# Kernel tuning notes

Hardware: AMD Instinct MI355X
Metric: run time of the kernel (lower is better)

Reference implementation:

```python
import jax, jax.numpy as jnp
import numpy as np
import math

E = 1024   # embedding_size
H = 16     # layer_size (num heads)
DK = 64    # key_size
DH = 64    # head_size
HID = 4096 # hidden_size
B = 2
S = 2048   # context_size
EPS = 1e-5


def layer_norm(x, w, b):
    mu = jnp.mean(x, axis=-1, keepdims=True)
    var = jnp.mean(jnp.square(x - mu), axis=-1, keepdims=True)
    return (x - mu) * jax.lax.rsqrt(var + EPS) * w + b


def setup_inputs() -> dict:
    key = jax.random.key(0)
    ks = jax.random.split(key, 16)
    sE = 1.0 / math.sqrt(E)
    sH = 1.0 / math.sqrt(HID)
    return {
        "embeddings": jax.random.normal(ks[0], (B, S, E), dtype=jnp.float32),
        "Wq": jax.random.uniform(ks[1], (H, E, DK), minval=-sE, maxval=sE, dtype=jnp.float32),
        "bq": jnp.zeros((H, DK), dtype=jnp.float32),
        "Wk": jax.random.uniform(ks[2], (H, E, DK), minval=-sE, maxval=sE, dtype=jnp.float32),
        "bk": jnp.zeros((H, DK), dtype=jnp.float32),
        "Wv": jax.random.uniform(ks[3], (H, E, DH), minval=-sE, maxval=sE, dtype=jnp.float32),
        "bv": jnp.zeros((H, DH), dtype=jnp.float32),
        "ln1_w": jnp.ones((E,), dtype=jnp.float32),
        "ln1_b": jnp.zeros((E,), dtype=jnp.float32),
        "ln2_w": jnp.ones((E,), dtype=jnp.float32),
        "ln2_b": jnp.zeros((E,), dtype=jnp.float32),
        "W1": jax.random.uniform(ks[4], (E, HID), minval=-sE, maxval=sE, dtype=jnp.float32),
        "b1": jnp.zeros((HID,), dtype=jnp.float32),
        "W2": jax.random.uniform(ks[5], (HID, E), minval=-sH, maxval=sH, dtype=jnp.float32),
        "b2": jnp.zeros((E,), dtype=jnp.float32),
    }


def reference(embeddings, Wq, bq, Wk, bk, Wv, bv, ln1_w, ln1_b, ln2_w, ln2_b, W1, b1, W2, b2):
    # NOTE: faithful to source: residual uses the POST-norm activations
    # (embeddings is reassigned to the LayerNorm output before the residual add).
    x = layer_norm(embeddings, ln1_w, ln1_b)            # [B,S,E]
    q = jnp.einsum('bse,hed->bhsd', x, Wq) + bq[:, None, :]
    k = jnp.einsum('bse,hed->bhsd', x, Wk) + bk[:, None, :]
    v = jnp.einsum('bse,hed->bhsd', x, Wv) + bv[:, None, :]
    scores = jnp.einsum('bhsd,bhtd->bhst', q, k) / math.sqrt(DK)  # [B,H,S,S]
    causal = jnp.tril(jnp.ones((S, S), dtype=bool))
    scores = jnp.where(causal, scores, -jnp.inf)
    w = jax.nn.softmax(scores, axis=-1)
    o = jnp.einsum('bhst,bhtd->bhsd', w, v)             # [B,H,S,DH]
    o = jnp.transpose(o, (0, 2, 1, 3)).reshape(B, S, H * DH)  # concat heads
    x = x + o
    y = layer_norm(x, ln2_w, ln2_b)
    h = jax.nn.relu(jnp.einsum('bse,eh->bsh', y, W1) + b1)
    out = y + jnp.einsum('bsh,he->bse', h, W2) + b2
    return out
```

## Files before the change

kernel.cpp:

```cpp
#include <hip/hip_runtime.h>


typedef unsigned short u16;
typedef unsigned int   u32;
typedef __bf16 bf16x8 __attribute__((ext_vector_type(8)));
typedef float  f32x4  __attribute__((ext_vector_type(4)));

#define NEG_INF (-__builtin_inff())

__device__ __forceinline__ u16 f2b(float f) {
  u32 u = __float_as_uint(f);
  u = (u + 0x7fffu + ((u >> 16) & 1u)) >> 16;
  return (u16)u;
}

__device__ __forceinline__ void gload16(const void* g, void* l) {
  __builtin_amdgcn_global_load_lds(
      (const __attribute__((address_space(1))) u32*)g,
      (__attribute__((address_space(3))) u32*)l, 16, 0, 0);
}

__global__ __launch_bounds__(256)
void transpose_bf16_k(const float* __restrict__ in, u16* __restrict__ out,
                      int R, int C) {
  __shared__ float tile[64][65];
  int r0 = blockIdx.x * 64, c0 = blockIdx.y * 64;
  const float* ip = in + (size_t)blockIdx.z * R * C;
  u16* op = out + (size_t)blockIdx.z * C * R;
  int tr = threadIdx.x >> 6, tc = threadIdx.x & 63;
#pragma unroll
  for (int i = 0; i < 16; i++) {
    int r = i * 4 + tr;
    tile[r][tc] = ip[(size_t)(r0 + r) * C + c0 + tc];
  }
  __syncthreads();
#pragma unroll
  for (int i = 0; i < 16; i++) {
    int c = i * 4 + tr;
    op[(size_t)(c0 + c) * R + r0 + tc] = f2b(tile[tc][c]);
  }
}

__global__ __launch_bounds__(256)
void vtrans_k(const u16* __restrict__ vin, u16* __restrict__ vt) {
  __shared__ __align__(16) u16 tile[64][72];
  int s0 = blockIdx.x * 64, bh = blockIdx.y;
  const u16* ip = vin + (size_t)bh * 2048 * 64;
  u16* op = vt + (size_t)bh * 64 * 2048;
  int t = threadIdx.x;
#pragma unroll
  for (int i = 0; i < 2; i++) {
    int idx = i * 256 + t, r = idx >> 3, c = idx & 7;
    *(uint4*)&tile[r][c * 8] = *(const uint4*)(ip + (size_t)(s0 + r) * 64 + c * 8);
  }
  __syncthreads();
#pragma unroll
  for (int i = 0; i < 16; i++) {
    int d = i * 4 + (t >> 6), s = t & 63;
    op[(size_t)d * 2048 + s0 + s] = tile[s][d];
  }
}

__global__ __launch_bounds__(256)
void ln_k(const float* __restrict__ in, const float* __restrict__ in2,
          const float* __restrict__ w, const float* __restrict__ b,
          float* __restrict__ outf, u16* __restrict__ outb) {
  int row = blockIdx.x, t = threadIdx.x;
  const float4* ip = (const float4*)(in + (size_t)row * 1024);
  float4 x = ip[t];
  if (in2) {
    const float4* ip2 = (const float4*)(in2 + (size_t)row * 1024);
    float4 o = ip2[t];
    x.x += o.x; x.y += o.y; x.z += o.z; x.w += o.w;
  }
  float s = x.x + x.y + x.z + x.w;
  float q = x.x * x.x + x.y * x.y + x.z * x.z + x.w * x.w;
#pragma unroll
  for (int m = 32; m; m >>= 1) { s += __shfl_xor(s, m); q += __shfl_xor(q, m); }
  __shared__ float rs[4], rq[4];
  if ((t & 63) == 0) { rs[t >> 6] = s; rq[t >> 6] = q; }
  __syncthreads();
  s = rs[0] + rs[1] + rs[2] + rs[3];
  q = rq[0] + rq[1] + rq[2] + rq[3];
  float mean = s * (1.f / 1024.f);
  float var  = q * (1.f / 1024.f) - mean * mean;
  float rstd = rsqrtf(var + 1e-5f);
  float4 wv = ((const float4*)w)[t];
  float4 bv = ((const float4*)b)[t];
  float4 y;
  y.x = (x.x - mean) * rstd * wv.x + bv.x;
  y.y = (x.y - mean) * rstd * wv.y + bv.y;
  y.z = (x.z - mean) * rstd * wv.z + bv.z;
  y.w = (x.w - mean) * rstd * wv.w + bv.w;
  if (outf) ((float4*)(outf + (size_t)row * 1024))[t] = y;
  ushort4 ub;
  ub.x = f2b(y.x); ub.y = f2b(y.y); ub.z = f2b(y.z); ub.w = f2b(y.w);
  ((ushort4*)(outb + (size_t)row * 1024))[t] = ub;
}

#define EPI_QKV  0
#define EPI_RELU 1
#define EPI_RES  2

template <int EPI>
__global__ __launch_bounds__(256)
void gemm_k(const u16* __restrict__ A, const u16* __restrict__ Bt,
            int K, int lda, int ldbt,
            const float* __restrict__ bias0, const float* __restrict__ bias1,
            const float* __restrict__ bias2, const float* __restrict__ res,
            int ldout, u16* __restrict__ outb, float* __restrict__ outf,
            float* __restrict__ outp) {
  __shared__ __align__(16) u16 As[128 * 64];
  __shared__ __align__(16) u16 Bs[128 * 64];
  int t = threadIdx.x;
  int wave = t >> 6, lane = t & 63, quad = lane >> 4, l16 = lane & 15;
  int x7 = l16 & 7;
  int wm = (wave >> 1) * 64, wn = (wave & 1) * 64;
  int bm = blockIdx.x * 128, bn = blockIdx.y * 128;
  int zoff = blockIdx.z * K;

  const u16* Agl[4];
  const u16* Bgl[4];
#pragma unroll
  for (int i = 0; i < 4; i++) {
    int idx = i * 256 + t, r = idx >> 3, c = (idx & 7) ^ (r & 7);
    Agl[i] = A + (size_t)(bm + r) * lda + zoff + c * 8;
    Bgl[i] = Bt + (size_t)(bn + r) * ldbt + zoff + c * 8;
  }
  u16* Asl = As + t * 8;
  u16* Bsl = Bs + t * 8;

  f32x4 acc[4][4] = {};

  for (int k0 = 0; k0 < K; k0 += 64) {
#pragma unroll
    for (int i = 0; i < 4; i++) {
      gload16(Agl[i] + k0, Asl + i * 2048);
      gload16(Bgl[i] + k0, Bsl + i * 2048);
    }
    __syncthreads();
#pragma unroll
    for (int kc = 0; kc < 2; kc++) {
      bf16x8 af[4], bfr[4];
#pragma unroll
      for (int i = 0; i < 4; i++) {
        int r = wm + i * 16 + l16;
        af[i] = *(const bf16x8*)(As + r * 64 + (((kc * 4 + quad) ^ x7) * 8));
      }
#pragma unroll
      for (int j = 0; j < 4; j++) {
        int r = wn + j * 16 + l16;
        bfr[j] = *(const bf16x8*)(Bs + r * 64 + (((kc * 4 + quad) ^ x7) * 8));
      }
#pragma unroll
      for (int i = 0; i < 4; i++)
#pragma unroll
        for (int j = 0; j < 4; j++)
          acc[i][j] = __builtin_amdgcn_mfma_f32_16x16x32_bf16(af[i], bfr[j],
                                                              acc[i][j], 0, 0, 0);
    }
    __syncthreads();
  }

#pragma unroll
  for (int i = 0; i < 4; i++) {
#pragma unroll
    for (int j = 0; j < 4; j++) {
      int c = bn + wn + j * 16 + l16;
#pragma unroll
      for (int rr = 0; rr < 4; rr++) {
        int r = bm + wm + i * 16 + quad * 4 + rr;
        float v = acc[i][j][rr];
        if (EPI == EPI_QKV) {
          int which = c >> 10, h = (c >> 6) & 15, d = c & 63;
          const float* bp = which == 0 ? bias0 : (which == 1 ? bias1 : bias2);
          v += bp[h * 64 + d];
          int bb = r >> 11, ss = r & 2047;
          outb[((size_t)(which * 32 + bb * 16 + h) * 2048 + ss) * 64 + d] = f2b(v);
        } else if (EPI == EPI_RELU) {
          v += bias0[c];
          v = v > 0.f ? v : 0.f;
          outb[(size_t)r * ldout + c] = f2b(v);
        } else {
          if (blockIdx.z == 0) {
            v += bias0[c] + res[(size_t)r * ldout + c];
            outf[(size_t)r * ldout + c] = v;
          } else {
            outp[(size_t)r * ldout + c] = v;
          }
        }
      }
    }
  }
}

__global__ __launch_bounds__(256)
void reduce_k(float* __restrict__ out, const float* __restrict__ part) {
  int i = blockIdx.x * 256 + threadIdx.x;
  float4 a = ((const float4*)part)[i];
  float4 b = ((float4*)out)[i];
  b.x += a.x; b.y += a.y; b.z += a.z; b.w += a.w;
  ((float4*)out)[i] = b;
}

__global__ __launch_bounds__(512, 4)
void attn_k(const u16* __restrict__ qkv, const u16* __restrict__ vt,
            float* __restrict__ o) {
  int bh = blockIdx.y;
  int Qt = (bh >> 4) ? (15 - (int)blockIdx.x) : (int)blockIdx.x;
  int b = bh >> 4, h = bh & 15;
  const u16* qg = qkv + (size_t)bh * (2048 * 64) + (size_t)Qt * 128 * 64;
  const u16* kg = qkv + (size_t)(32 + bh) * (2048 * 64);
  const u16* vg = vt + (size_t)bh * (64 * 2048);

  __shared__ __align__(16) u16 Qs[128 * 64];
  __shared__ __align__(16) u16 Ks[2][64 * 64];
  __shared__ __align__(16) u16 Vs[2][64 * 64];
  __shared__ __align__(16) u16 Ps[8][16 * 64];

  int t = threadIdx.x;
  int wave = t >> 6, lane = t & 63, quad = lane >> 4, l16 = lane & 15;

  {
#pragma unroll
    for (int i = 0; i < 2; i++) {
      int idx = i * 512 + t, r = idx >> 3, c = (idx & 7) ^ (r & 7);
      gload16(qg + r * 64 + c * 8, Qs + idx * 8);
    }
    int r = t >> 3, c = (t & 7) ^ (r & 7);
    gload16(kg + (size_t)r * 64 + c * 8, Ks[0] + t * 8);
    gload16(vg + (size_t)r * 2048 + c * 8, Vs[0] + t * 8);
  }
  __syncthreads();

  int x7 = l16 & 7;
  bf16x8 qf[2];
  {
    const u16* qr = Qs + (wave * 16 + l16) * 64;
    qf[0] = *(const bf16x8*)(qr + ((quad ^ x7) * 8));
    qf[1] = *(const bf16x8*)(qr + (((4 + quad) ^ x7) * 8));
  }

  f32x4 oacc[4] = {};
  float mo[4] = {NEG_INF, NEG_INF, NEG_INF, NEG_INF};
  float ll[4] = {};
  u16* Pw = Ps[wave];
  int rmin = Qt * 128 + wave * 16;
  int kmax_w = (rmin + 15) >> 6;
  int klast = 2 * Qt + 1;

  for (int kt = 0; kt <= klast; kt++) {
    const u16* ks = Ks[kt & 1];
    const u16* vs = Vs[kt & 1];
    if (kt < klast) {
      int r = t >> 3, c = (t & 7) ^ (r & 7);
      gload16(kg + (size_t)((kt + 1) * 64 + r) * 64 + c * 8, Ks[(kt + 1) & 1] + t * 8);
      gload16(vg + (size_t)r * 2048 + (kt + 1) * 64 + c * 8, Vs[(kt + 1) & 1] + t * 8);
    }
    if (kt <= kmax_w) {
      f32x4 sc[4];
#pragma unroll
      for (int g = 0; g < 4; g++) {
        const u16* kr = ks + (g * 16 + l16) * 64;
        bf16x8 kf0 = *(const bf16x8*)(kr + ((quad ^ x7) * 8));
        bf16x8 kf1 = *(const bf16x8*)(kr + (((4 + quad) ^ x7) * 8));
        f32x4 s = {};
        s = __builtin_amdgcn_mfma_f32_16x16x32_bf16(qf[0], kf0, s, 0, 0, 0);
        s = __builtin_amdgcn_mfma_f32_16x16x32_bf16(qf[1], kf1, s, 0, 0, 0);
        sc[g] = s;
      }
      if (kt * 64 + 63 > rmin) {
#pragma unroll
        for (int g = 0; g < 4; g++) {
          int col = kt * 64 + g * 16 + l16;
#pragma unroll
          for (int rr = 0; rr < 4; rr++) {
            int row = rmin + quad * 4 + rr;
            sc[g][rr] = (col <= row) ? sc[g][rr] * 0.125f : NEG_INF;
          }
        }
      } else {
#pragma unroll
        for (int g = 0; g < 4; g++)
#pragma unroll
          for (int rr = 0; rr < 4; rr++) sc[g][rr] *= 0.125f;
      }
      float al[4], rsum[4];
#pragma unroll
      for (int rr = 0; rr < 4; rr++) {
        float mx = fmaxf(fmaxf(sc[0][rr], sc[1][rr]), fmaxf(sc[2][rr], sc[3][rr]));
        mx = fmaxf(mx, __shfl_xor(mx, 1));
        mx = fmaxf(mx, __shfl_xor(mx, 2));
        mx = fmaxf(mx, __shfl_xor(mx, 4));
        mx = fmaxf(mx, __shfl_xor(mx, 8));
        float mnew = fmaxf(mo[rr], mx);
        al[rr] = __expf(mo[rr] - mnew);
        mo[rr] = mnew;
        rsum[rr] = 0.f;
      }
#pragma unroll
      for (int g = 0; g < 4; g++) {
        int cbase = (g * 16 + l16 + quad * 16) & 63;
#pragma unroll
        for (int rr = 0; rr < 4; rr++) {
          float p = __expf(sc[g][rr] - mo[rr]);
          rsum[rr] += p;
          Pw[(quad * 4 + rr) * 64 + cbase] = f2b(p);
        }
      }
#pragma unroll
      for (int rr = 0; rr < 4; rr++) {
        rsum[rr] += __shfl_xor(rsum[rr], 1);
        rsum[rr] += __shfl_xor(rsum[rr], 2);
        rsum[rr] += __shfl_xor(rsum[rr], 4);
        rsum[rr] += __shfl_xor(rsum[rr], 8);
        ll[rr] = ll[rr] * al[rr] + rsum[rr];
      }
#pragma unroll
      for (int g = 0; g < 4; g++)
#pragma unroll
        for (int rr = 0; rr < 4; rr++) oacc[g][rr] *= al[rr];
      bf16x8 pf0, pf1;
      {
        const u16* pr = Pw + l16 * 64;
        int sh = (l16 & 12) * 4;
        pf0 = *(const bf16x8*)(pr + ((quad * 8 + sh) & 63));
        pf1 = *(const bf16x8*)(pr + ((32 + quad * 8 + sh) & 63));
      }
#pragma unroll
      for (int g = 0; g < 4; g++) {
        const u16* vr = vs + (g * 16 + l16) * 64;
        bf16x8 vf0 = *(const bf16x8*)(vr + ((quad ^ x7) * 8));
        bf16x8 vf1 = *(const bf16x8*)(vr + (((4 + quad) ^ x7) * 8));
        oacc[g] = __builtin_amdgcn_mfma_f32_16x16x32_bf16(pf0, vf0, oacc[g], 0, 0, 0);
        oacc[g] = __builtin_amdgcn_mfma_f32_16x16x32_bf16(pf1, vf1, oacc[g], 0, 0, 0);
      }
    }
    __syncthreads();
  }

#pragma unroll
  for (int g = 0; g < 4; g++)
#pragma unroll
    for (int rr = 0; rr < 4; rr++) {
      int srow = rmin + quad * 4 + rr;
      o[((size_t)b * 2048 + srow) * 1024 + h * 64 + g * 16 + l16] =
          oacc[g][rr] / ll[rr];
    }
}

extern "C" void kernel_launch(void* const* d_in, const int* in_sizes, int n_in,
                              void* d_out, int out_size, void* d_ws, size_t ws_size,
                              hipStream_t stream) {
  const float* emb  = (const float*)d_in[0];
  const float* Wq   = (const float*)d_in[1];
  const float* bq   = (const float*)d_in[2];
  const float* Wk   = (const float*)d_in[3];
  const float* bk   = (const float*)d_in[4];
  const float* Wv   = (const float*)d_in[5];
  const float* bv   = (const float*)d_in[6];
  const float* ln1w = (const float*)d_in[7];
  const float* ln1b = (const float*)d_in[8];
  const float* ln2w = (const float*)d_in[9];
  const float* ln2b = (const float*)d_in[10];
  const float* W1   = (const float*)d_in[11];
  const float* b1   = (const float*)d_in[12];
  const float* W2   = (const float*)d_in[13];
  const float* b2   = (const float*)d_in[14];
  float* out = (float*)d_out;

  char* p = (char*)d_ws;
  u16*   Wqkv_t = (u16*)p;   p += (size_t)3072 * 1024 * 2;
  u16*   W1t    = (u16*)p;   p += (size_t)4096 * 1024 * 2;
  u16*   W2t    = (u16*)p;   p += (size_t)1024 * 4096 * 2;
  float* x      = (float*)p; p += (size_t)4096 * 1024 * 4;
  u16*   xb     = (u16*)p;   p += (size_t)4096 * 1024 * 2;
  u16*   qkvb   = (u16*)p;   p += (size_t)3 * 32 * 2048 * 64 * 2;
  float* ob     = (float*)p; p += (size_t)4096 * 1024 * 4;
  float* y      = (float*)p; p += (size_t)4096 * 1024 * 4;
  u16*   yb     = (u16*)p;   p += (size_t)4096 * 1024 * 2;
  u16*   hb     = (u16*)qkvb;
  u16*   vT     = (u16*)y;
  float* part   = x;
  if (ws_size < (size_t)(p - (char*)d_ws)) return;

  transpose_bf16_k<<<dim3(16, 1, 16), 256, 0, stream>>>(Wq, Wqkv_t,                   1024, 64);
  transpose_bf16_k<<<dim3(16, 1, 16), 256, 0, stream>>>(Wk, Wqkv_t + 1024 * 1024,     1024, 64);
  transpose_bf16_k<<<dim3(16, 1, 16), 256, 0, stream>>>(Wv, Wqkv_t + 2 * 1024 * 1024, 1024, 64);
  transpose_bf16_k<<<dim3(16, 64, 1), 256, 0, stream>>>(W1, W1t, 1024, 4096);
  transpose_bf16_k<<<dim3(64, 16, 1), 256, 0, stream>>>(W2, W2t, 4096, 1024);

  ln_k<<<dim3(4096), 256, 0, stream>>>(emb, nullptr, ln1w, ln1b, x, xb);

  gemm_k<EPI_QKV><<<dim3(32, 24, 1), 256, 0, stream>>>(
      xb, Wqkv_t, 1024, 1024, 1024, bq, bk, bv, nullptr, 0, qkvb, nullptr, nullptr);

  vtrans_k<<<dim3(32, 32), 256, 0, stream>>>(qkvb + (size_t)64 * 2048 * 64, vT);

  attn_k<<<dim3(16, 32), 512, 0, stream>>>(qkvb, vT, ob);

  ln_k<<<dim3(4096), 256, 0, stream>>>(x, ob, ln2w, ln2b, y, yb);

  gemm_k<EPI_RELU><<<dim3(32, 32, 1), 256, 0, stream>>>(
      yb, W1t, 1024, 1024, 1024, b1, nullptr, nullptr, nullptr, 4096, hb, nullptr, nullptr);

  gemm_k<EPI_RES><<<dim3(32, 8, 2), 256, 0, stream>>>(
      hb, W2t, 2048, 4096, 4096, b2, nullptr, nullptr, y, 1024, nullptr, out, part);

  reduce_k<<<dim3(4096), 256, 0, stream>>>(out, part);
}
```

Baseline: 359.4 us.

## Restructure attention to read K/V directly from global with transposed score tiles

The attention kernel drops the shared-memory double-buffered K/V staging and block-wide barriers. Each 16-row wave now loads Q, K and V fragments straight from global memory, relying on cache reuse. Scores are computed transposed (K as the A operand), so row max and sum need only two cross-lane shuffles, and exp2 is used with the softmax scale times log2(e) folded into the Q projection epilogue. Blocks shrink to 64 query rows and 256 threads over a larger grid, which adds redundant global/L2 traffic for K/V in exchange for no LDS staging or synchronisation.

```diff
diff --git a/kernel.cpp b/kernel.cpp
--- a/kernel.cpp
+++ b/kernel.cpp
@@ -8,6 +8,12 @@
 
 #define NEG_INF (-__builtin_inff())
 
+#if __has_builtin(__builtin_amdgcn_exp2f)
+#define EXP2F(x) __builtin_amdgcn_exp2f(x)
+#else
+#define EXP2F(x) exp2f(x)
+#endif
+
 __device__ __forceinline__ u16 f2b(float f) {
   u32 u = __float_as_uint(f);
   u = (u + 0x7fffu + ((u >> 16) & 1u)) >> 16;
@@ -19,6 +25,8 @@
       (const __attribute__((address_space(1))) u32*)g,
       (__attribute__((address_space(3))) u32*)l, 16, 0, 0);
 }
+
+__device__ __forceinline__ bf16x8 ld16(const u16* p) { return *(const bf16x8*)p; }
 
 __global__ __launch_bounds__(256)
 void transpose_bf16_k(const float* __restrict__ in, u16* __restrict__ out,
@@ -102,6 +110,8 @@
 #define EPI_RELU 1
 #define EPI_RES  2
 
+#define QSCALE 0.18033688011112042f
+
 template <int EPI>
 __global__ __launch_bounds__(256)
 void gemm_k(const u16* __restrict__ A, const u16* __restrict__ Bt,
@@ -175,6 +185,7 @@
           int which = c >> 10, h = (c >> 6) & 15, d = c & 63;
           const float* bp = which == 0 ? bias0 : (which == 1 ? bias1 : bias2);
           v += bp[h * 64 + d];
+          if (which == 0) v *= QSCALE;
           int bb = r >> 11, ss = r & 2047;
           outb[((size_t)(which * 32 + bb * 16 + h) * 2048 + ss) * 64 + d] = f2b(v);
         } else if (EPI == EPI_RELU) {
@@ -203,150 +214,110 @@
   ((float4*)out)[i] = b;
 }
 
-__global__ __launch_bounds__(512, 4)
+__global__ __launch_bounds__(256)
 void attn_k(const u16* __restrict__ qkv, const u16* __restrict__ vt,
             float* __restrict__ o) {
-  int bh = blockIdx.y;
-  int Qt = (bh >> 4) ? (15 - (int)blockIdx.x) : (int)blockIdx.x;
-  int b = bh >> 4, h = bh & 15;
-  const u16* qg = qkv + (size_t)bh * (2048 * 64) + (size_t)Qt * 128 * 64;
+  int bh = blockIdx.y, b = bh >> 4, h = bh & 15;
+  int xt = b ? (31 - (int)blockIdx.x) : (int)blockIdx.x;
+  int t = threadIdx.x;
+  int wave = t >> 6, lane = t & 63, quad = lane >> 4, l16 = lane & 15;
+  int x7 = l16 & 7;
+  int q0 = xt * 64 + wave * 16;
+
+  const u16* qg = qkv + (size_t)bh * (2048 * 64);
   const u16* kg = qkv + (size_t)(32 + bh) * (2048 * 64);
   const u16* vg = vt + (size_t)bh * (64 * 2048);
 
-  __shared__ __align__(16) u16 Qs[128 * 64];
-  __shared__ __align__(16) u16 Ks[2][64 * 64];
-  __shared__ __align__(16) u16 Vs[2][64 * 64];
-  __shared__ __align__(16) u16 Ps[8][16 * 64];
-
-  int t = threadIdx.x;
-  int wave = t >> 6, lane = t & 63, quad = lane >> 4, l16 = lane & 15;
-
-  {
-#pragma unroll
-    for (int i = 0; i < 2; i++) {
-      int idx = i * 512 + t, r = idx >> 3, c = (idx & 7) ^ (r & 7);
-      gload16(qg + r * 64 + c * 8, Qs + idx * 8);
-    }
-    int r = t >> 3, c = (t & 7) ^ (r & 7);
-    gload16(kg + (size_t)r * 64 + c * 8, Ks[0] + t * 8);
-    gload16(vg + (size_t)r * 2048 + c * 8, Vs[0] + t * 8);
-  }
-  __syncthreads();
-
-  int x7 = l16 & 7;
-  bf16x8 qf[2];
-  {
-    const u16* qr = Qs + (wave * 16 + l16) * 64;
-    qf[0] = *(const bf16x8*)(qr + ((quad ^ x7) * 8));
-    qf[1] = *(const bf16x8*)(qr + (((4 + quad) ^ x7) * 8));
-  }
+  __shared__ __align__(16) u16 Ps[4][16 * 64];
+  u16* Pw = Ps[wave];
+
+  bf16x8 qf0 = ld16(qg + (size_t)(q0 + l16) * 64 + quad * 8);
+  bf16x8 qf1 = ld16(qg + (size_t)(q0 + l16) * 64 + 32 + quad * 8);
 
   f32x4 oacc[4] = {};
-  float mo[4] = {NEG_INF, NEG_INF, NEG_INF, NEG_INF};
-  float ll[4] = {};
-  u16* Pw = Ps[wave];
-  int rmin = Qt * 128 + wave * 16;
-  int kmax_w = (rmin + 15) >> 6;
-  int klast = 2 * Qt + 1;
-
-  for (int kt = 0; kt <= klast; kt++) {
-    const u16* ks = Ks[kt & 1];
-    const u16* vs = Vs[kt & 1];
-    if (kt < klast) {
-      int r = t >> 3, c = (t & 7) ^ (r & 7);
-      gload16(kg + (size_t)((kt + 1) * 64 + r) * 64 + c * 8, Ks[(kt + 1) & 1] + t * 8);
-      gload16(vg + (size_t)r * 2048 + (kt + 1) * 64 + c * 8, Vs[(kt + 1) & 1] + t * 8);
-    }
-    if (kt <= kmax_w) {
-      f32x4 sc[4];
+  float mo = NEG_INF, ll = 0.f;
+  int kmax = (q0 + 15) >> 6;
+
+  for (int kt = 0; kt <= kmax; kt++) {
+    const u16* kb = kg + (size_t)kt * 64 * 64;
+    const u16* vb = vg + (size_t)kt * 64;
+
+    f32x4 sc[4];
+#pragma unroll
+    for (int g = 0; g < 4; g++) {
+      bf16x8 kf0 = ld16(kb + (size_t)(g * 16 + l16) * 64 + quad * 8);
+      bf16x8 kf1 = ld16(kb + (size_t)(g * 16 + l16) * 64 + 32 + quad * 8);
+      f32x4 s = {};
+      s = __builtin_amdgcn_mfma_f32_16x16x32_bf16(kf0, qf0, s, 0, 0, 0);
+      s = __builtin_amdgcn_mfma_f32_16x16x32_bf16(kf1, qf1, s, 0, 0, 0);
+      sc[g] = s;
+    }
+
+    if (kt == kmax) {
 #pragma unroll
       for (int g = 0; g < 4; g++) {
-        const u16* kr = ks + (g * 16 + l16) * 64;
-        bf16x8 kf0 = *(const bf16x8*)(kr + ((quad ^ x7) * 8));
-        bf16x8 kf1 = *(const bf16x8*)(kr + (((4 + quad) ^ x7) * 8));
-        f32x4 s = {};
-        s = __builtin_amdgcn_mfma_f32_16x16x32_bf16(qf[0], kf0, s, 0, 0, 0);
-        s = __builtin_amdgcn_mfma_f32_16x16x32_bf16(qf[1], kf1, s, 0, 0, 0);
-        sc[g] = s;
+        int kvb = kt * 64 + g * 16 + quad * 4;
+#pragma unroll
+        for (int rr = 0; rr < 4; rr++)
+          if (kvb + rr > q0 + l16) sc[g][rr] = NEG_INF;
       }
-      if (kt * 64 + 63 > rmin) {
-#pragma unroll
-        for (int g = 0; g < 4; g++) {
-          int col = kt * 64 + g * 16 + l16;
-#pragma unroll
-          for (int rr = 0; rr < 4; rr++) {
-            int row = rmin + quad * 4 + rr;
-            sc[g][rr] = (col <= row) ? sc[g][rr] * 0.125f : NEG_INF;
-          }
-        }
-      } else {
-#pragma unroll
-        for (int g = 0; g < 4; g++)
-#pragma unroll
-          for (int rr = 0; rr < 4; rr++) sc[g][rr] *= 0.125f;
-      }
-      float al[4], rsum[4];
-#pragma unroll
-      for (int rr = 0; rr < 4; rr++) {
-        float mx = fmaxf(fmaxf(sc[0][rr], sc[1][rr]), fmaxf(sc[2][rr], sc[3][rr]));
-        mx = fmaxf(mx, __shfl_xor(mx, 1));
-        mx = fmaxf(mx, __shfl_xor(mx, 2));
-        mx = fmaxf(mx, __shfl_xor(mx, 4));
-        mx = fmaxf(mx, __shfl_xor(mx, 8));
-        float mnew = fmaxf(mo[rr], mx);
-        al[rr] = __expf(mo[rr] - mnew);
-        mo[rr] = mnew;
-        rsum[rr] = 0.f;
-      }
-#pragma unroll
-      for (int g = 0; g < 4; g++) {
-        int cbase = (g * 16 + l16 + quad * 16) & 63;
-#pragma unroll
-        for (int rr = 0; rr < 4; rr++) {
-          float p = __expf(sc[g][rr] - mo[rr]);
-          rsum[rr] += p;
-          Pw[(quad * 4 + rr) * 64 + cbase] = f2b(p);
-        }
-      }
-#pragma unroll
-      for (int rr = 0; rr < 4; rr++) {
-        rsum[rr] += __shfl_xor(rsum[rr], 1);
-        rsum[rr] += __shfl_xor(rsum[rr], 2);
-        rsum[rr] += __shfl_xor(rsum[rr], 4);
-        rsum[rr] += __shfl_xor(rsum[rr], 8);
-        ll[rr] = ll[rr] * al[rr] + rsum[rr];
-      }
-#pragma unroll
-      for (int g = 0; g < 4; g++)
-#pragma unroll
-        for (int rr = 0; rr < 4; rr++) oacc[g][rr] *= al[rr];
-      bf16x8 pf0, pf1;
-      {
-        const u16* pr = Pw + l16 * 64;
-        int sh = (l16 & 12) * 4;
-        pf0 = *(const bf16x8*)(pr + ((quad * 8 + sh) & 63));
-        pf1 = *(const bf16x8*)(pr + ((32 + quad * 8 + sh) & 63));
-      }
-#pragma unroll
-      for (int g = 0; g < 4; g++) {
-        const u16* vr = vs + (g * 16 + l16) * 64;
-        bf16x8 vf0 = *(const bf16x8*)(vr + ((quad ^ x7) * 8));
-        bf16x8 vf1 = *(const bf16x8*)(vr + (((4 + quad) ^ x7) * 8));
-        oacc[g] = __builtin_amdgcn_mfma_f32_16x16x32_bf16(pf0, vf0, oacc[g], 0, 0, 0);
-        oacc[g] = __builtin_amdgcn_mfma_f32_16x16x32_bf16(pf1, vf1, oacc[g], 0, 0, 0);
-      }
-    }
-    __syncthreads();
-  }
-
+    }
+
+    float mx = sc[0][0];
+#pragma unroll
+    for (int g = 0; g < 4; g++)
+#pragma unroll
+      for (int rr = 0; rr < 4; rr++) mx = fmaxf(mx, sc[g][rr]);
+    mx = fmaxf(mx, __shfl_xor(mx, 16));
+    mx = fmaxf(mx, __shfl_xor(mx, 32));
+    float mnew = fmaxf(mo, mx);
+    float al = EXP2F(mo - mnew);
+    mo = mnew;
+
+    float sum = 0.f;
+#pragma unroll
+    for (int g = 0; g < 4; g++) {
+      float p0 = EXP2F(sc[g][0] - mnew);
+      float p1 = EXP2F(sc[g][1] - mnew);
+      float p2 = EXP2F(sc[g][2] - mnew);
+      float p3 = EXP2F(sc[g][3] - mnew);
+      sum += (p0 + p1) + (p2 + p3);
+      u32 lo = (__float_as_uint(p0) >> 16) | (__float_as_uint(p1) & 0xFFFF0000u);
+      u32 hi = (__float_as_uint(p2) >> 16) | (__float_as_uint(p3) & 0xFFFF0000u);
+      int slot = (2 * g + (quad >> 1)) ^ x7;
+      *(uint2*)(Pw + l16 * 64 + slot * 8 + (quad & 1) * 4) = make_uint2(lo, hi);
+    }
+    sum += __shfl_xor(sum, 16);
+    sum += __shfl_xor(sum, 32);
+    ll = ll * al + sum;
+
+#pragma unroll
+    for (int rr = 0; rr < 4; rr++) {
+      float ar = __shfl(al, quad * 20 + rr);
+#pragma unroll
+      for (int g = 0; g < 4; g++) oacc[g][rr] *= ar;
+    }
+
+    bf16x8 pf0 = *(const bf16x8*)(Pw + l16 * 64 + ((quad ^ x7) * 8));
+    bf16x8 pf1 = *(const bf16x8*)(Pw + l16 * 64 + (((4 + quad) ^ x7) * 8));
+#pragma unroll
+    for (int g = 0; g < 4; g++) {
+      bf16x8 vf0 = ld16(vb + (size_t)(g * 16 + l16) * 2048 + quad * 8);
+      bf16x8 vf1 = ld16(vb + (size_t)(g * 16 + l16) * 2048 + 32 + quad * 8);
+      oacc[g] = __builtin_amdgcn_mfma_f32_16x16x32_bf16(pf0, vf0, oacc[g], 0, 0, 0);
+      oacc[g] = __builtin_amdgcn_mfma_f32_16x16x32_bf16(pf1, vf1, oacc[g], 0, 0, 0);
+    }
+  }
+
+  float rinv[4];
+#pragma unroll
+  for (int rr = 0; rr < 4; rr++) rinv[rr] = 1.f / __shfl(ll, quad * 20 + rr);
+  float* op = o + ((size_t)b * 2048 + q0) * 1024 + h * 64;
 #pragma unroll
   for (int g = 0; g < 4; g++)
 #pragma unroll
-    for (int rr = 0; rr < 4; rr++) {
-      int srow = rmin + quad * 4 + rr;
-      o[((size_t)b * 2048 + srow) * 1024 + h * 64 + g * 16 + l16] =
-          oacc[g][rr] / ll[rr];
-    }
+    for (int rr = 0; rr < 4; rr++)
+      op[(size_t)(quad * 4 + rr) * 1024 + g * 16 + l16] = oacc[g][rr] * rinv[rr];
 }
 
 extern "C" void kernel_launch(void* const* d_in, const int* in_sizes, int n_in,
@@ -397,7 +368,7 @@
 
   vtrans_k<<<dim3(32, 32), 256, 0, stream>>>(qkvb + (size_t)64 * 2048 * 64, vT);
 
-  attn_k<<<dim3(16, 32), 512, 0, stream>>>(qkvb, vT, ob);
+  attn_k<<<dim3(32, 32), 256, 0, stream>>>(qkvb, vT, ob);
 
   ln_k<<<dim3(4096), 256, 0, stream>>>(x, ob, ln2w, ln2b, y, yb);
 
```

After: 423.5 us. +17.8%, slower.
